# Kernel optimization log

Hardware: AMD Instinct MI355X
Metric: run time of the kernel (lower is better)

## Reference

```python
import jax, jax.numpy as jnp
import numpy as np

DIM = 1024
NUM_HEADS = 16
DIM_HEAD = 64
INNER = NUM_HEADS * DIM_HEAD  # 1024
SCALE = DIM_HEAD ** -0.5


def setup_inputs() -> dict:
    key = jax.random.key(0)
    ks = jax.random.split(key, 8)
    B, SQ, SK = 2, 2048, 4096
    x = jax.random.normal(ks[0], (B, SQ, DIM), dtype=jnp.float32)
    context = jax.random.normal(ks[1], (B, SK, DIM), dtype=jnp.float32)
    # LayerNorm params
    ln_gamma = jnp.ones((DIM,), jnp.float32)
    ln_beta = jnp.zeros((DIM,), jnp.float32)
    # Linear weights, stored as [in, out] so y = x @ W (torch Linear weight transposed)
    w_q = jax.random.normal(ks[2], (DIM, INNER), dtype=jnp.float32) / np.sqrt(DIM)
    w_kv = jax.random.normal(ks[3], (DIM, 2 * INNER), dtype=jnp.float32) / np.sqrt(DIM)
    w_out = jax.random.normal(ks[4], (INNER, DIM), dtype=jnp.float32) / np.sqrt(INNER)
    b_out = jnp.zeros((DIM,), jnp.float32)
    # torch init is 0.0 (tanh(0)=0); use a nonzero value so output/grads are nontrivial
    gate = jnp.array([0.5], jnp.float32)
    return {"x": x, "context": context, "ln_gamma": ln_gamma, "ln_beta": ln_beta,
            "w_q": w_q, "w_kv": w_kv, "w_out": w_out, "b_out": b_out, "gate": gate}


def _layernorm(x, gamma, beta, eps=1e-5):
    mu = jnp.mean(x, axis=-1, keepdims=True)
    var = jnp.mean(jnp.square(x - mu), axis=-1, keepdims=True)
    return (x - mu) * jax.lax.rsqrt(var + eps) * gamma + beta


def reference(x, context, ln_gamma, ln_beta, w_q, w_kv, w_out, b_out, gate):
    B, SQ, _ = x.shape
    SK = context.shape[1]
    xn = _layernorm(x, ln_gamma, ln_beta)
    q = (xn @ w_q).reshape(B, SQ, NUM_HEADS, DIM_HEAD)
    kv = context @ w_kv
    k, v = jnp.split(kv, 2, axis=-1)
    k = k.reshape(B, SK, NUM_HEADS, DIM_HEAD)
    v = v.reshape(B, SK, NUM_HEADS, DIM_HEAD)
    # scores: [B, H, SQ, SK]
    scores = jnp.einsum('bqhd,bkhd->bhqk', q * SCALE, k)
    attn = jax.nn.softmax(scores, axis=-1)
    out = jnp.einsum('bhqk,bkhd->bqhd', attn, v).reshape(B, SQ, INNER)
    out = out @ w_out + b_out
    return out * jnp.tanh(gate[0])
```

## Files before the change

### kernel.cpp

```cpp
#include <hip/hip_runtime.h>
#include <hip/hip_bf16.h>
#include <stdint.h>

#define DIMM  1024
#define NHEAD 16
#define DHEAD 64
#define BB    2
#define SQL   2048
#define SKL   4096
#define KVW   2048

typedef __attribute__((ext_vector_type(8))) short short8;
typedef __attribute__((ext_vector_type(4))) float f32x4;
typedef __attribute__((ext_vector_type(4))) unsigned short us4;

typedef const __attribute__((address_space(1))) uint32_t gu32_t;
typedef __attribute__((address_space(3))) uint32_t lu32_t;

#define GLDS16(gp, lp) __builtin_amdgcn_global_load_lds((gu32_t*)(gp), (lu32_t*)(lp), 16, 0, 0)

static __device__ __forceinline__ unsigned short f2bf(float f) {
  union { float f; uint32_t u; } v; v.f = f;
  uint32_t r = v.u + 0x7fffu + ((v.u >> 16) & 1u);
  return (unsigned short)(r >> 16);
}

__global__ __launch_bounds__(256) void k_transpose_cast(const float* __restrict__ in,
                                                        unsigned short* __restrict__ out,
                                                        int K, int N) {
  __shared__ float tile[32][33];
  int n0 = blockIdx.x * 32, k0 = blockIdx.y * 32;
  int tx = threadIdx.x, ty = threadIdx.y;
  #pragma unroll
  for (int i = 0; i < 4; i++)
    tile[ty + i * 8][tx] = in[(size_t)(k0 + ty + i * 8) * N + n0 + tx];
  __syncthreads();
  #pragma unroll
  for (int i = 0; i < 4; i++)
    out[(size_t)(n0 + ty + i * 8) * K + k0 + tx] = f2bf(tile[tx][ty + i * 8]);
}

__global__ __launch_bounds__(256) void k_cast(const float* __restrict__ in,
                                              unsigned short* __restrict__ out) {
  size_t i = (size_t)(blockIdx.x * 256 + threadIdx.x) * 4;
  float4 v = *(const float4*)(in + i);
  us4 o;
  o.x = f2bf(v.x); o.y = f2bf(v.y); o.z = f2bf(v.z); o.w = f2bf(v.w);
  *(us4*)(out + i) = o;
}

__global__ __launch_bounds__(256) void k_ln(const float* __restrict__ x,
                                            const float* __restrict__ gamma,
                                            const float* __restrict__ beta,
                                            unsigned short* __restrict__ out) {
  const int row = blockIdx.x, tid = threadIdx.x;
  const float* xr = x + (size_t)row * DIMM;
  float4 v = *(const float4*)(xr + tid * 4);
  float s = v.x + v.y + v.z + v.w;
  float ss = v.x * v.x + v.y * v.y + v.z * v.z + v.w * v.w;
  #pragma unroll
  for (int m = 1; m < 64; m <<= 1) {
    s += __shfl_xor(s, m);
    ss += __shfl_xor(ss, m);
  }
  __shared__ float red[8];
  const int wid = tid >> 6, lane = tid & 63;
  if (lane == 0) { red[wid] = s; red[4 + wid] = ss; }
  __syncthreads();
  s = red[0] + red[1] + red[2] + red[3];
  ss = red[4] + red[5] + red[6] + red[7];
  float mu = s * (1.0f / DIMM);
  float var = ss * (1.0f / DIMM) - mu * mu;
  float rstd = rsqrtf(var + 1e-5f);
  float4 g = *(const float4*)(gamma + tid * 4);
  float4 bt = *(const float4*)(beta + tid * 4);
  us4 o;
  o.x = f2bf((v.x - mu) * rstd * g.x + bt.x);
  o.y = f2bf((v.y - mu) * rstd * g.y + bt.y);
  o.z = f2bf((v.z - mu) * rstd * g.z + bt.z);
  o.w = f2bf((v.w - mu) * rstd * g.w + bt.w);
  *(us4*)(out + (size_t)row * DIMM + tid * 4) = o;
}

template<int MODE>
__global__ __launch_bounds__(256) void k_gemm_bt(const unsigned short* __restrict__ A,
                                                 const unsigned short* __restrict__ BT,
                                                 void* __restrict__ Cv,
                                                 int M, int N, int K,
                                                 const float* __restrict__ bias,
                                                 const float* __restrict__ gate) {
  __shared__ unsigned short lA[2][128 * 32];
  __shared__ unsigned short lB[2][128 * 32];
  const int tid = threadIdx.x;
  const int wid = tid >> 6, lane = tid & 63;
  const int kg = lane >> 4, lr = lane & 15;
  const int wr = wid >> 1, wc = wid & 1;
  const int im = blockIdx.x, in_ = blockIdx.y;
  const int nt = K >> 5;
  const size_t baseA = (size_t)im * 128 * K;
  const size_t baseB = (size_t)in_ * 128 * K;

  f32x4 acc[4][4];
  #pragma unroll
  for (int m = 0; m < 4; m++)
    #pragma unroll
    for (int n = 0; n < 4; n++) {
      f32x4 z = {0.0f, 0.0f, 0.0f, 0.0f};
      acc[m][n] = z;
    }

  auto GSTAGE = [&](int bufi, int t) {
    int k0 = t << 5;
    #pragma unroll
    for (int j = 0; j < 2; j++) {
      int e = wid * 1024 + j * 512 + lane * 8;
      int row = e >> 5;
      int g = (e >> 3) & 3;
      int col = (g ^ ((row >> 1) & 3)) << 3;
      GLDS16(A + baseA + (size_t)row * K + k0 + col, &lA[bufi][e]);
      GLDS16(BT + baseB + (size_t)row * K + k0 + col, &lB[bufi][e]);
    }
  };

  GSTAGE(0, 0);
  __syncthreads();
  int buf = 0;
  for (int t = 0; t < nt; t++) {
    if (t + 1 < nt) GSTAGE(buf ^ 1, t + 1);
    short8 a[4], b[4];
    #pragma unroll
    for (int m = 0; m < 4; m++) {
      int row = wr * 64 + m * 16 + lr;
      a[m] = *(const short8*)&lA[buf][row * 32 + ((kg ^ ((row >> 1) & 3)) << 3)];
    }
    #pragma unroll
    for (int n = 0; n < 4; n++) {
      int row = wc * 64 + n * 16 + lr;
      b[n] = *(const short8*)&lB[buf][row * 32 + ((kg ^ ((row >> 1) & 3)) << 3)];
    }
    #pragma unroll
    for (int m = 0; m < 4; m++)
      #pragma unroll
      for (int n = 0; n < 4; n++)
        acc[m][n] = __builtin_amdgcn_mfma_f32_16x16x32_bf16(a[m], b[n], acc[m][n], 0, 0, 0);
    __syncthreads();
    buf ^= 1;
  }

  const int r0 = im * 128 + wr * 64;
  const int c0 = in_ * 128 + wc * 64;
  if constexpr (MODE == 0) {
    unsigned short* C = (unsigned short*)Cv;
    #pragma unroll
    for (int m = 0; m < 4; m++)
      #pragma unroll
      for (int n = 0; n < 4; n++)
        #pragma unroll
        for (int j = 0; j < 4; j++)
          C[(size_t)(r0 + m * 16 + kg * 4 + j) * N + c0 + n * 16 + lr] = f2bf(acc[m][n][j]);
  } else {
    float* C = (float*)Cv;
    float gl = tanhf(gate[0]);
    #pragma unroll
    for (int m = 0; m < 4; m++)
      #pragma unroll
      for (int n = 0; n < 4; n++)
        #pragma unroll
        for (int j = 0; j < 4; j++) {
          int col = c0 + n * 16 + lr;
          C[(size_t)(r0 + m * 16 + kg * 4 + j) * N + col] = (acc[m][n][j] + bias[col]) * gl;
        }
  }
}

__global__ __launch_bounds__(256, 2) void k_attn(const unsigned short* __restrict__ Q,
                                                 const unsigned short* __restrict__ KV,
                                                 unsigned short* __restrict__ O) {
  __shared__ unsigned short sK[2][64 * 64];
  __shared__ unsigned short sVT[2][64 * 64];
  __shared__ unsigned short sP[4][2][16 * 72];

  const int tid = threadIdx.x;
  const int wid = tid >> 6, lane = tid & 63;
  const int kg = lane >> 4, lr = lane & 15;
  const int qb = blockIdx.x, bh = blockIdx.y;
  const int b = bh >> 4, h = bh & 15;

  const unsigned short* Qp = Q + (size_t)b * SQL * DIMM + h * DHEAD;
  const unsigned short* Kp = KV + (size_t)b * SKL * KVW + h * DHEAD;
  const unsigned short* Vp = Kp + DIMM;

  const int qr0 = qb * 128 + wid * 32;

  short8 qa[2][2];
  #pragma unroll
  for (int m = 0; m < 2; m++)
    #pragma unroll
    for (int ks = 0; ks < 2; ks++) {
      short8 v = *(const short8*)(Qp + (size_t)(qr0 + m * 16 + lr) * DIMM + ks * 32 + kg * 8);
      #pragma unroll
      for (int j = 0; j < 8; j++) {
        union { float f; uint32_t u; } c;
        c.u = ((uint32_t)(unsigned short)v[j]) << 16;
        v[j] = (short)f2bf(c.f * 0.1803368801111f);
      }
      qa[m][ks] = v;
    }

  f32x4 oacc[2][4];
  #pragma unroll
  for (int m = 0; m < 2; m++)
    #pragma unroll
    for (int n = 0; n < 4; n++) {
      f32x4 z = {0.0f, 0.0f, 0.0f, 0.0f};
      oacc[m][n] = z;
    }
  float rs[2] = {0.0f, 0.0f};

  const int keyr = tid >> 2;
  const int vd0 = (tid & 3) * 16;
  short8 vv[2];

  auto STAGE_K = [&](int bufi, int kt) {
    #pragma unroll
    for (int j = 0; j < 2; j++) {
      int e = wid * 1024 + j * 512 + lane * 8;
      int row = e >> 6;
      int g = (e >> 3) & 7;
      int col = (g ^ (row & 7)) << 3;
      GLDS16(Kp + (size_t)(kt * 64 + row) * KVW + col, &sK[bufi][e]);
    }
  };
  auto LOAD_V = [&](int kt) {
    #pragma unroll
    for (int c = 0; c < 2; c++)
      vv[c] = *(const short8*)(Vp + (size_t)(kt * 64 + keyr) * KVW + vd0 + c * 8);
  };
  auto STORE_V = [&](int bufi) {
    #pragma unroll
    for (int c = 0; c < 2; c++)
      #pragma unroll
      for (int j = 0; j < 8; j++) {
        int d = vd0 + c * 8 + j;
        int hd = (d & 7) ^ ((d >> 3) & 7);
        sVT[bufi][d * 64 + (keyr ^ (hd << 3))] = (unsigned short)vv[c][j];
      }
  };

  LOAD_V(0);
  STAGE_K(0, 0);
  STORE_V(0);
  __syncthreads();

  int buf = 0;
  for (int kt = 0; kt < SKL / 64; kt++) {
    const bool more = (kt + 1 < SKL / 64);
    if (more) { LOAD_V(kt + 1); STAGE_K(buf ^ 1, kt + 1); }

    short8 kb[4][2];
    #pragma unroll
    for (int n = 0; n < 4; n++)
      #pragma unroll
      for (int ks = 0; ks < 2; ks++) {
        int row = n * 16 + lr;
        kb[n][ks] = *(const short8*)&sK[buf][row * 64 + (((ks * 4 + kg) ^ (row & 7)) << 3)];
      }
    f32x4 sc[4][2];
    #pragma unroll
    for (int n = 0; n < 4; n++)
      #pragma unroll
      for (int m = 0; m < 2; m++) {
        f32x4 z = {0.0f, 0.0f, 0.0f, 0.0f};
        sc[n][m] = z;
      }
    #pragma unroll
    for (int n = 0; n < 4; n++)
      #pragma unroll
      for (int m = 0; m < 2; m++)
        #pragma unroll
        for (int ks = 0; ks < 2; ks++)
          sc[n][m] = __builtin_amdgcn_mfma_f32_16x16x32_bf16(kb[n][ks], qa[m][ks], sc[n][m], 0, 0, 0);

    #pragma unroll
    for (int m = 0; m < 2; m++) {
      unsigned short* sPw = &sP[wid][m][0];
      #pragma unroll
      for (int n = 0; n < 4; n++) {
        float p0 = __builtin_amdgcn_exp2f(sc[n][m][0]);
        float p1 = __builtin_amdgcn_exp2f(sc[n][m][1]);
        float p2 = __builtin_amdgcn_exp2f(sc[n][m][2]);
        float p3 = __builtin_amdgcn_exp2f(sc[n][m][3]);
        rs[m] += (p0 + p1) + (p2 + p3);
        us4 w;
        w.x = f2bf(p0); w.y = f2bf(p1); w.z = f2bf(p2); w.w = f2bf(p3);
        *(us4*)&sPw[lr * 72 + n * 16 + kg * 4] = w;
      }
    }

    asm volatile("" ::: "memory");

    short8 pa[2][2], vb[4][2];
    #pragma unroll
    for (int m = 0; m < 2; m++)
      #pragma unroll
      for (int ks2 = 0; ks2 < 2; ks2++)
        pa[m][ks2] = *(const short8*)&sP[wid][m][lr * 72 + ks2 * 32 + kg * 8];
    #pragma unroll
    for (int n = 0; n < 4; n++)
      #pragma unroll
      for (int ks2 = 0; ks2 < 2; ks2++) {
        int d = n * 16 + lr;
        int hd = (d & 7) ^ ((d >> 3) & 7);
        vb[n][ks2] = *(const short8*)&sVT[buf][d * 64 + (((ks2 * 4 + kg) ^ hd) << 3)];
      }
    #pragma unroll
    for (int m = 0; m < 2; m++)
      #pragma unroll
      for (int n = 0; n < 4; n++)
        #pragma unroll
        for (int ks2 = 0; ks2 < 2; ks2++)
          oacc[m][n] = __builtin_amdgcn_mfma_f32_16x16x32_bf16(pa[m][ks2], vb[n][ks2], oacc[m][n], 0, 0, 0);

    if (more) STORE_V(buf ^ 1);
    __syncthreads();
    buf ^= 1;
  }

  float inv[2];
  #pragma unroll
  for (int m = 0; m < 2; m++) {
    float t = rs[m];
    t += __shfl_xor(t, 16);
    t += __shfl_xor(t, 32);
    inv[m] = 1.0f / t;
  }
  float rq[2][4];
  #pragma unroll
  for (int m = 0; m < 2; m++)
    #pragma unroll
    for (int j = 0; j < 4; j++)
      rq[m][j] = __shfl(inv[m], kg * 4 + j);

  unsigned short* Op = O + (size_t)b * SQL * DIMM + h * DHEAD;
  #pragma unroll
  for (int m = 0; m < 2; m++)
    #pragma unroll
    for (int n = 0; n < 4; n++)
      #pragma unroll
      for (int j = 0; j < 4; j++)
        Op[(size_t)(qr0 + m * 16 + kg * 4 + j) * DIMM + n * 16 + lr] =
            f2bf(oacc[m][n][j] * rq[m][j]);
}

extern "C" void kernel_launch(void* const* d_in, const int* in_sizes, int n_in,
                              void* d_out, int out_size, void* d_ws, size_t ws_size,
                              hipStream_t stream) {
  (void)in_sizes; (void)n_in; (void)out_size; (void)ws_size;
  const float* x     = (const float*)d_in[0];
  const float* ctx   = (const float*)d_in[1];
  const float* gamma = (const float*)d_in[2];
  const float* beta  = (const float*)d_in[3];
  const float* w_q   = (const float*)d_in[4];
  const float* w_kv  = (const float*)d_in[5];
  const float* w_out = (const float*)d_in[6];
  const float* b_out = (const float*)d_in[7];
  const float* gate  = (const float*)d_in[8];
  float* out = (float*)d_out;
  char* ws = (char*)d_ws;

  unsigned short* XN   = (unsigned short*)(ws);
  unsigned short* QB   = (unsigned short*)(ws + (8ull  << 20));
  unsigned short* CTXB = (unsigned short*)(ws + (16ull << 20));
  unsigned short* KVB  = (unsigned short*)(ws + (32ull << 20));
  unsigned short* OB   = (unsigned short*)(ws + (64ull << 20));
  unsigned short* WQT  = (unsigned short*)(ws + (72ull << 20));
  unsigned short* WKVT = (unsigned short*)(ws + (74ull << 20));
  unsigned short* WOT  = (unsigned short*)(ws + (78ull << 20));

  k_transpose_cast<<<dim3(32, 32), dim3(32, 8), 0, stream>>>(w_q, WQT, 1024, 1024);
  k_transpose_cast<<<dim3(64, 32), dim3(32, 8), 0, stream>>>(w_kv, WKVT, 1024, 2048);
  k_transpose_cast<<<dim3(32, 32), dim3(32, 8), 0, stream>>>(w_out, WOT, 1024, 1024);
  k_cast<<<dim3(8192), dim3(256), 0, stream>>>(ctx, CTXB);
  k_ln<<<dim3(4096), dim3(256), 0, stream>>>(x, gamma, beta, XN);
  k_gemm_bt<0><<<dim3(32, 8), dim3(256), 0, stream>>>(XN, WQT, QB, 4096, 1024, 1024, nullptr, nullptr);
  k_gemm_bt<0><<<dim3(64, 16), dim3(256), 0, stream>>>(CTXB, WKVT, KVB, 8192, 2048, 1024, nullptr, nullptr);
  k_attn<<<dim3(16, 32), dim3(256), 0, stream>>>(QB, KVB, OB);
  k_gemm_bt<1><<<dim3(32, 8), dim3(256), 0, stream>>>(OB, WOT, out, 4096, 1024, 1024, b_out, gate);
}
```

Before: 247.5 us.

## Load V tiles directly to LDS and read transposed via ds_read_b64_tr_b16

Replaces the register-staged V load plus scalar transposed LDS stores with direct global-to-LDS async copies in a key-interleaved layout. The PV MFMA operand is then read with the hardware transpose-read instruction. Separately, P is packed to bf16 with the native v_cvt_pk_bf16_f32 instead of software rounding. This is meant to remove many per-element LDS writes and VGPR pressure from the V path. In exchange it adds an explicit lgkmcnt wait and a scheduling barrier that may limit overlap, and it relies on correct inline-asm layout assumptions.

New measurement: 236.6 us. -4.4%, faster.

```diff
diff --git a/kernel.cpp b/kernel.cpp
--- a/kernel.cpp
+++ b/kernel.cpp
@@ -177,7 +177,7 @@
                                                  const unsigned short* __restrict__ KV,
                                                  unsigned short* __restrict__ O) {
   __shared__ unsigned short sK[2][64 * 64];
-  __shared__ unsigned short sVT[2][64 * 64];
+  __shared__ unsigned short sV[2][64 * 64];
   __shared__ unsigned short sP[4][2][16 * 72];
 
   const int tid = threadIdx.x;
@@ -217,45 +217,44 @@
     }
   float rs[2] = {0.0f, 0.0f};
 
-  const int keyr = tid >> 2;
-  const int vd0 = (tid & 3) * 16;
-  short8 vv[2];
-
-  auto STAGE_K = [&](int bufi, int kt) {
-    #pragma unroll
-    for (int j = 0; j < 2; j++) {
-      int e = wid * 1024 + j * 512 + lane * 8;
-      int row = e >> 6;
-      int g = (e >> 3) & 7;
-      int col = (g ^ (row & 7)) << 3;
-      GLDS16(Kp + (size_t)(kt * 64 + row) * KVW + col, &sK[bufi][e]);
-    }
+  const unsigned short* ksrc[2]; int kdst[2];
+  #pragma unroll
+  for (int j = 0; j < 2; j++) {
+    int e = wid * 1024 + j * 512 + lane * 8;
+    int row = e >> 6;
+    int col = (((e >> 3) & 7) ^ (row & 7)) << 3;
+    ksrc[j] = Kp + (size_t)row * KVW + col;
+    kdst[j] = e;
+  }
+  const unsigned short* vsrc[2]; int vdst[2];
+  #pragma unroll
+  for (int j = 0; j < 2; j++) {
+    int g = tid + j * 256;
+    int key = (g >> 5) * 4 + ((g & 7) >> 1);
+    int d0v = ((g >> 3) & 3) * 16 + (g & 1) * 8;
+    vsrc[j] = Vp + (size_t)key * KVW + d0v;
+    vdst[j] = g * 8;
+  }
+
+  auto STAGE = [&](int bufi, int kt) {
+    size_t off = (size_t)kt * 64 * KVW;
+    #pragma unroll
+    for (int j = 0; j < 2; j++) GLDS16(ksrc[j] + off, &sK[bufi][kdst[j]]);
+    #pragma unroll
+    for (int j = 0; j < 2; j++) GLDS16(vsrc[j] + off, &sV[bufi][vdst[j]]);
   };
-  auto LOAD_V = [&](int kt) {
-    #pragma unroll
-    for (int c = 0; c < 2; c++)
-      vv[c] = *(const short8*)(Vp + (size_t)(kt * 64 + keyr) * KVW + vd0 + c * 8);
-  };
-  auto STORE_V = [&](int bufi) {
-    #pragma unroll
-    for (int c = 0; c < 2; c++)
-      #pragma unroll
-      for (int j = 0; j < 8; j++) {
-        int d = vd0 + c * 8 + j;
-        int hd = (d & 7) ^ ((d >> 3) & 7);
-        sVT[bufi][d * 64 + (keyr ^ (hd << 3))] = (unsigned short)vv[c][j];
-      }
-  };
-
-  LOAD_V(0);
-  STAGE_K(0, 0);
-  STORE_V(0);
+
+  uint32_t sVbase[2];
+  sVbase[0] = (uint32_t)(size_t)(lu32_t*)&sV[0][0] + (uint32_t)(kg * 1024 + lr * 8);
+  sVbase[1] = (uint32_t)(size_t)(lu32_t*)&sV[1][0] + (uint32_t)(kg * 1024 + lr * 8);
+
+  STAGE(0, 0);
   __syncthreads();
 
   int buf = 0;
   for (int kt = 0; kt < SKL / 64; kt++) {
     const bool more = (kt + 1 < SKL / 64);
-    if (more) { LOAD_V(kt + 1); STAGE_K(buf ^ 1, kt + 1); }
+    if (more) STAGE(buf ^ 1, kt + 1);
 
     short8 kb[4][2];
     #pragma unroll
@@ -291,37 +290,49 @@
         float p2 = __builtin_amdgcn_exp2f(sc[n][m][2]);
         float p3 = __builtin_amdgcn_exp2f(sc[n][m][3]);
         rs[m] += (p0 + p1) + (p2 + p3);
-        us4 w;
-        w.x = f2bf(p0); w.y = f2bf(p1); w.z = f2bf(p2); w.w = f2bf(p3);
-        *(us4*)&sPw[lr * 72 + n * 16 + kg * 4] = w;
+        uint32_t lo, hi;
+        asm("v_cvt_pk_bf16_f32 %0, %1, %2" : "=v"(lo) : "v"(p0), "v"(p1));
+        asm("v_cvt_pk_bf16_f32 %0, %1, %2" : "=v"(hi) : "v"(p2), "v"(p3));
+        uint2 w2; w2.x = lo; w2.y = hi;
+        *(uint2*)&sPw[lr * 72 + n * 16 + kg * 4] = w2;
       }
     }
 
     asm volatile("" ::: "memory");
 
-    short8 pa[2][2], vb[4][2];
+    short8 pa[2][2];
     #pragma unroll
     for (int m = 0; m < 2; m++)
       #pragma unroll
       for (int ks2 = 0; ks2 < 2; ks2++)
         pa[m][ks2] = *(const short8*)&sP[wid][m][lr * 72 + ks2 * 32 + kg * 8];
-    #pragma unroll
-    for (int n = 0; n < 4; n++)
-      #pragma unroll
-      for (int ks2 = 0; ks2 < 2; ks2++) {
-        int d = n * 16 + lr;
-        int hd = (d & 7) ^ ((d >> 3) & 7);
-        vb[n][ks2] = *(const short8*)&sVT[buf][d * 64 + (((ks2 * 4 + kg) ^ hd) << 3)];
-      }
+
+    union { uint4 u; short8 s; } vbu[4][2];
+    {
+      uint32_t tb = sVbase[buf];
+      #pragma unroll
+      for (int n = 0; n < 4; n++)
+        #pragma unroll
+        for (int ks2 = 0; ks2 < 2; ks2++) {
+          uint2 t0, t1;
+          uint32_t a0 = tb + (uint32_t)(ks2 * 4096 + n * 128);
+          asm volatile("ds_read_b64_tr_b16 %0, %1" : "=v"(t0) : "v"(a0));
+          asm volatile("ds_read_b64_tr_b16 %0, %1" : "=v"(t1) : "v"(a0 + 512u));
+          vbu[n][ks2].u.x = t0.x; vbu[n][ks2].u.y = t0.y;
+          vbu[n][ks2].u.z = t1.x; vbu[n][ks2].u.w = t1.y;
+        }
+    }
+    asm volatile("s_waitcnt lgkmcnt(0)" ::: "memory");
+    __builtin_amdgcn_sched_barrier(0);
+
     #pragma unroll
     for (int m = 0; m < 2; m++)
       #pragma unroll
       for (int n = 0; n < 4; n++)
         #pragma unroll
         for (int ks2 = 0; ks2 < 2; ks2++)
-          oacc[m][n] = __builtin_amdgcn_mfma_f32_16x16x32_bf16(pa[m][ks2], vb[n][ks2], oacc[m][n], 0, 0, 0);
-
-    if (more) STORE_V(buf ^ 1);
+          oacc[m][n] = __builtin_amdgcn_mfma_f32_16x16x32_bf16(pa[m][ks2], vbu[n][ks2].s, oacc[m][n], 0, 0, 0);
+
     __syncthreads();
     buf ^= 1;
   }
```
